# Kernel optimization log

Hardware: AMD Instinct MI355X
Metric: run time of the kernel (lower is better)

The kernel has to match this reference:

```python
import jax, jax.numpy as jnp
import numpy as np

MUL = 32          # channel multiplicity of every irrep
N_NODES = 50000
N_EDGES = 800000
SQRT2 = 1.4142135623730951
SQRT3 = 1.7320508075688772


def setup_inputs() -> dict:
    key = jax.random.key(0)
    k1, k2, k3, k4, k5 = jax.random.split(key, 5)
    x = jax.random.normal(k1, (N_NODES, 4 * MUL), dtype=jnp.float32)          # 32x0e + 32x1o
    edge_attr = jax.random.normal(k2, (N_EDGES, 4), dtype=jnp.float32)        # 1x0e + 1x1o
    edge_weight = jax.random.normal(k3, (N_EDGES, 5 * MUL), dtype=jnp.float32)  # 5 uvu paths
    edge_dst = jax.random.randint(k4, (N_EDGES,), 0, N_NODES, dtype=jnp.int64)
    edge_src = jax.random.randint(k5, (N_EDGES,), 0, N_NODES, dtype=jnp.int64)
    return {"x": x, "edge_attr": edge_attr, "edge_weight": edge_weight,
            "edge_dst": edge_dst, "edge_src": edge_src}


def _tp_scatter(x, edge_attr, edge_weight, edge_dst, edge_src):
    N = x.shape[0]
    E = edge_attr.shape[0]
    # split node features into l=0 scalars and l=1 vectors
    x0 = x[:, :MUL]                              # [N, 32]
    x1 = x[:, MUL:].reshape(N, MUL, 3)           # [N, 32, 3]
    a0 = edge_attr[:, :1]                        # [E, 1]
    a1 = edge_attr[:, 1:4]                       # [E, 3]
    w0, w1, w2, w3, w4 = [edge_weight[:, i * MUL:(i + 1) * MUL] for i in range(5)]

    xs0 = x0[edge_src]                           # [E, 32]  gather
    xs1 = x1[edge_src]                           # [E, 32, 3]

    # path 1: 0e x 0e -> 0e   (CG = 1, alpha = 1)
    o0 = w0 * xs0 * a0                                                   # [E, 32]
    # path 2: 0e x 1o -> 1o   (CG = delta/sqrt3, alpha = sqrt3 => net 1)
    o1 = (w1 * xs0)[:, :, None] * a1[:, None, :]                         # [E, 32, 3]
    # path 3: 1o x 0e -> 1o   (net coefficient 1)
    o2 = (w2[:, :, None] * xs1) * a0[:, :, None]                         # [E, 32, 3]
    # path 4: 1o x 1o -> 0e   (CG = delta/sqrt3, alpha = 1 => net 1/sqrt3)
    o3 = w3 * jnp.einsum('euk,ek->eu', xs1, a1) / SQRT3                  # [E, 32]
    # path 5: 1o x 1o -> 1e   (CG = eps/sqrt6, alpha = sqrt3 => net 1/sqrt2)
    o4 = w4[:, :, None] * jnp.cross(xs1, a1[:, None, :]) / SQRT2         # [E, 32, 3]

    edge_features = jnp.concatenate(
        [o0, o1.reshape(E, -1), o2.reshape(E, -1), o3, o4.reshape(E, -1)], axis=1)  # [E, 352]
    # scatter-add to destination nodes
    return jax.ops.segment_sum(edge_features, edge_dst, num_segments=N)  # [N, 352]


def reference(x, edge_attr, edge_weight, edge_dst, edge_src):
    return _tp_scatter(x, edge_attr, edge_weight, edge_dst, edge_src)
```

## Files before the change

### kernel.cpp

```cpp
#include <hip/hip_runtime.h>

#define MUL 32
#define N_NODES 50000
#define N_EDGES 800000
#define ROW_OUT 352
#define ROW_X 128
#define ROW_W 160

#define INV_SQRT3 0.57735026918962576f
#define INV_SQRT2 0.70710678118654752f

#define SCAN_THREADS 1024

__global__ __launch_bounds__(256) void hist_kernel(
    const int* __restrict__ edge_dst, int* __restrict__ counts)
{
    int e = blockIdx.x * blockDim.x + threadIdx.x;
    if (e < N_EDGES) atomicAdd(&counts[edge_dst[e]], 1);
}

__global__ __launch_bounds__(SCAN_THREADS) void scan_kernel(
    const int* __restrict__ counts, int* __restrict__ offsets,
    int* __restrict__ cursor)
{
    __shared__ int lds[SCAN_THREADS];
    const int t = threadIdx.x;
    int carry = 0;
    for (int base = 0; base < N_NODES; base += SCAN_THREADS) {
        int i = base + t;
        int v = (i < N_NODES) ? counts[i] : 0;
        lds[t] = v;
        __syncthreads();
        for (int off = 1; off < SCAN_THREADS; off <<= 1) {
            int add = (t >= off) ? lds[t - off] : 0;
            __syncthreads();
            lds[t] += add;
            __syncthreads();
        }
        int incl = lds[t];
        int excl = incl - v + carry;
        if (i < N_NODES) { offsets[i] = excl; cursor[i] = excl; }
        carry += lds[SCAN_THREADS - 1];
        __syncthreads();
    }
}

__global__ __launch_bounds__(256) void fill_kernel(
    const int* __restrict__ edge_dst, int* __restrict__ cursor,
    int* __restrict__ edge_ids)
{
    int e = blockIdx.x * blockDim.x + threadIdx.x;
    if (e < N_EDGES) {
        int p = atomicAdd(&cursor[edge_dst[e]], 1);
        edge_ids[p] = e;
    }
}

__global__ __launch_bounds__(256) void gather_kernel(
    const float* __restrict__ x,
    const float* __restrict__ edge_attr,
    const float* __restrict__ edge_weight,
    const int*   __restrict__ edge_src,
    const int*   __restrict__ offsets,
    const int*   __restrict__ counts,
    const int*   __restrict__ edge_ids,
    float*       __restrict__ out)
{
    const int wave_in_block = threadIdx.x >> 6;
    const int n = blockIdx.x * (blockDim.x >> 6) + wave_in_block;
    if (n >= N_NODES) return;

    const int lane = threadIdx.x & 63;
    const int half = lane >> 5;
    const int u = lane & 31;

    const int start = offsets[n];
    const int deg = counts[n];

    float acc0 = 0.f;
    float acc1x = 0.f, acc1y = 0.f, acc1z = 0.f;
    float acc2x = 0.f, acc2y = 0.f, acc2z = 0.f;
    float acc3 = 0.f;
    float acc4x = 0.f, acc4y = 0.f, acc4z = 0.f;

    for (int j = half; j < deg; j += 2) {
        const int e = edge_ids[start + j];
        const int src = edge_src[e];

        const float4 a = *reinterpret_cast<const float4*>(edge_attr + (size_t)e * 4);
        const float a0  = a.x;
        const float a1x = a.y, a1y = a.z, a1z = a.w;

        const float* wrow = edge_weight + (size_t)e * ROW_W;
        const float w0 = wrow[0 * MUL + u];
        const float w1 = wrow[1 * MUL + u];
        const float w2 = wrow[2 * MUL + u];
        const float w3 = wrow[3 * MUL + u];
        const float w4 = wrow[4 * MUL + u];

        const float* xrow = x + (size_t)src * ROW_X;
        const float xs0 = xrow[u];
        const float x1x = xrow[MUL + u * 3 + 0];
        const float x1y = xrow[MUL + u * 3 + 1];
        const float x1z = xrow[MUL + u * 3 + 2];

        acc0 += w0 * xs0 * a0;

        const float w1xs0 = w1 * xs0;
        acc1x += w1xs0 * a1x;
        acc1y += w1xs0 * a1y;
        acc1z += w1xs0 * a1z;

        const float w2a0 = w2 * a0;
        acc2x += w2a0 * x1x;
        acc2y += w2a0 * x1y;
        acc2z += w2a0 * x1z;

        const float dot = x1x * a1x + x1y * a1y + x1z * a1z;
        acc3 += w3 * dot * INV_SQRT3;

        const float cx = x1y * a1z - x1z * a1y;
        const float cy = x1z * a1x - x1x * a1z;
        const float cz = x1x * a1y - x1y * a1x;
        const float w4s = w4 * INV_SQRT2;
        acc4x += w4s * cx;
        acc4y += w4s * cy;
        acc4z += w4s * cz;
    }

    acc0  += __shfl_down(acc0, 32);
    acc1x += __shfl_down(acc1x, 32);
    acc1y += __shfl_down(acc1y, 32);
    acc1z += __shfl_down(acc1z, 32);
    acc2x += __shfl_down(acc2x, 32);
    acc2y += __shfl_down(acc2y, 32);
    acc2z += __shfl_down(acc2z, 32);
    acc3  += __shfl_down(acc3, 32);
    acc4x += __shfl_down(acc4x, 32);
    acc4y += __shfl_down(acc4y, 32);
    acc4z += __shfl_down(acc4z, 32);

    if (half == 0) {
        float* orow = out + (size_t)n * ROW_OUT;
        orow[u] = acc0;
        orow[1 * MUL + u * 3 + 0] = acc1x;
        orow[1 * MUL + u * 3 + 1] = acc1y;
        orow[1 * MUL + u * 3 + 2] = acc1z;
        orow[4 * MUL + u * 3 + 0] = acc2x;
        orow[4 * MUL + u * 3 + 1] = acc2y;
        orow[4 * MUL + u * 3 + 2] = acc2z;
        orow[7 * MUL + u] = acc3;
        orow[8 * MUL + u * 3 + 0] = acc4x;
        orow[8 * MUL + u * 3 + 1] = acc4y;
        orow[8 * MUL + u * 3 + 2] = acc4z;
    }
}

extern "C" void kernel_launch(void* const* d_in, const int* in_sizes, int n_in,
                              void* d_out, int out_size, void* d_ws, size_t ws_size,
                              hipStream_t stream) {
    const float* x           = (const float*)d_in[0];
    const float* edge_attr   = (const float*)d_in[1];
    const float* edge_weight = (const float*)d_in[2];
    const int*   edge_dst    = (const int*)d_in[3];
    const int*   edge_src    = (const int*)d_in[4];
    float* out = (float*)d_out;

    int* counts   = (int*)d_ws;
    int* offsets  = counts + N_NODES;
    int* cursor   = offsets + N_NODES;
    int* edge_ids = cursor + N_NODES;

    hipMemsetAsync(counts, 0, (size_t)N_NODES * sizeof(int), stream);

    const int eb = (N_EDGES + 255) / 256;
    hist_kernel<<<eb, 256, 0, stream>>>(edge_dst, counts);
    scan_kernel<<<1, SCAN_THREADS, 0, stream>>>(counts, offsets, cursor);
    fill_kernel<<<eb, 256, 0, stream>>>(edge_dst, cursor, edge_ids);

    const int waves_per_block = 4;
    const int nb = (N_NODES + waves_per_block - 1) / waves_per_block;
    gather_kernel<<<nb, waves_per_block * 64, 0, stream>>>(
        x, edge_attr, edge_weight, edge_src, offsets, counts, edge_ids, out);
}
```

Measured before the change: 914.9 us.

## Prefetch next edge, pack edge/src pairs, and use wave-shuffle scan

The single-block scan now uses wave-level shuffle scans with a small per-wave combine, replacing the LDS Hillis-Steele loop full of barriers, and it prefetches the next chunk of counts. The fill kernel stores (edge id, src) pairs, so the gather no longer does a dependent edge_src lookup. The gather loop software-pipelines by loading the next edge's data while computing the current one, and it reads edge weights with nontemporal loads. This costs more registers, which may lower occupancy.

```diff
diff --git a/kernel.cpp b/kernel.cpp
--- a/kernel.cpp
+++ b/kernel.cpp
@@ -23,47 +23,101 @@
     const int* __restrict__ counts, int* __restrict__ offsets,
     int* __restrict__ cursor)
 {
-    __shared__ int lds[SCAN_THREADS];
+    __shared__ int wsum[16];
+    __shared__ int wexcl[16];
+    __shared__ int blocktot;
+
     const int t = threadIdx.x;
+    const int w = t >> 6;
+    const int lane = t & 63;
+
     int carry = 0;
+    int v = (t < N_NODES) ? counts[t] : 0;
+
     for (int base = 0; base < N_NODES; base += SCAN_THREADS) {
-        int i = base + t;
-        int v = (i < N_NODES) ? counts[i] : 0;
-        lds[t] = v;
+        const int inext = base + SCAN_THREADS + t;
+        int vnext = (inext < N_NODES) ? counts[inext] : 0;
+
+        int s = v;
+        #pragma unroll
+        for (int off = 1; off < 64; off <<= 1) {
+            int y = __shfl_up(s, off);
+            if (lane >= off) s += y;
+        }
+        if (lane == 63) wsum[w] = s;
         __syncthreads();
-        for (int off = 1; off < SCAN_THREADS; off <<= 1) {
-            int add = (t >= off) ? lds[t - off] : 0;
-            __syncthreads();
-            lds[t] += add;
-            __syncthreads();
+
+        if (t < 16) {
+            int ws_ = wsum[t];
+            int ss = ws_;
+            #pragma unroll
+            for (int off = 1; off < 16; off <<= 1) {
+                int y = __shfl_up(ss, off);
+                if (t >= off) ss += y;
+            }
+            wexcl[t] = ss - ws_;
+            if (t == 15) blocktot = ss;
         }
-        int incl = lds[t];
-        int excl = incl - v + carry;
+        __syncthreads();
+
+        const int excl = s - v + wexcl[w] + carry;
+        const int i = base + t;
         if (i < N_NODES) { offsets[i] = excl; cursor[i] = excl; }
-        carry += lds[SCAN_THREADS - 1];
+        carry += blocktot;
+        v = vnext;
         __syncthreads();
     }
 }
 
 __global__ __launch_bounds__(256) void fill_kernel(
-    const int* __restrict__ edge_dst, int* __restrict__ cursor,
-    int* __restrict__ edge_ids)
+    const int* __restrict__ edge_dst, const int* __restrict__ edge_src,
+    int* __restrict__ cursor, int2* __restrict__ pairs)
 {
     int e = blockIdx.x * blockDim.x + threadIdx.x;
     if (e < N_EDGES) {
         int p = atomicAdd(&cursor[edge_dst[e]], 1);
-        edge_ids[p] = e;
-    }
+        pairs[p] = make_int2(e, edge_src[e]);
+    }
+}
+
+struct Ed {
+    float a0, a1x, a1y, a1z;
+    float w0, w1, w2, w3, w4;
+    float xs0, x1x, x1y, x1z;
+};
+
+__device__ __forceinline__ Ed load_edge(
+    const float* __restrict__ x,
+    const float* __restrict__ edge_attr,
+    const float* __restrict__ edge_weight,
+    int2 p, int u)
+{
+    Ed d;
+    const float4 a = *reinterpret_cast<const float4*>(edge_attr + (size_t)p.x * 4);
+    d.a0 = a.x; d.a1x = a.y; d.a1y = a.z; d.a1z = a.w;
+
+    const float* wrow = edge_weight + (size_t)p.x * ROW_W;
+    d.w0 = __builtin_nontemporal_load(wrow + 0 * MUL + u);
+    d.w1 = __builtin_nontemporal_load(wrow + 1 * MUL + u);
+    d.w2 = __builtin_nontemporal_load(wrow + 2 * MUL + u);
+    d.w3 = __builtin_nontemporal_load(wrow + 3 * MUL + u);
+    d.w4 = __builtin_nontemporal_load(wrow + 4 * MUL + u);
+
+    const float* xrow = x + (size_t)p.y * ROW_X;
+    d.xs0 = xrow[u];
+    d.x1x = xrow[MUL + u * 3 + 0];
+    d.x1y = xrow[MUL + u * 3 + 1];
+    d.x1z = xrow[MUL + u * 3 + 2];
+    return d;
 }
 
 __global__ __launch_bounds__(256) void gather_kernel(
     const float* __restrict__ x,
     const float* __restrict__ edge_attr,
     const float* __restrict__ edge_weight,
-    const int*   __restrict__ edge_src,
     const int*   __restrict__ offsets,
     const int*   __restrict__ counts,
-    const int*   __restrict__ edge_ids,
+    const int2*  __restrict__ pairs,
     float*       __restrict__ out)
 {
     const int wave_in_block = threadIdx.x >> 6;
@@ -83,49 +137,42 @@
     float acc3 = 0.f;
     float acc4x = 0.f, acc4y = 0.f, acc4z = 0.f;
 
-    for (int j = half; j < deg; j += 2) {
-        const int e = edge_ids[start + j];
-        const int src = edge_src[e];
-
-        const float4 a = *reinterpret_cast<const float4*>(edge_attr + (size_t)e * 4);
-        const float a0  = a.x;
-        const float a1x = a.y, a1y = a.z, a1z = a.w;
-
-        const float* wrow = edge_weight + (size_t)e * ROW_W;
-        const float w0 = wrow[0 * MUL + u];
-        const float w1 = wrow[1 * MUL + u];
-        const float w2 = wrow[2 * MUL + u];
-        const float w3 = wrow[3 * MUL + u];
-        const float w4 = wrow[4 * MUL + u];
-
-        const float* xrow = x + (size_t)src * ROW_X;
-        const float xs0 = xrow[u];
-        const float x1x = xrow[MUL + u * 3 + 0];
-        const float x1y = xrow[MUL + u * 3 + 1];
-        const float x1z = xrow[MUL + u * 3 + 2];
-
-        acc0 += w0 * xs0 * a0;
-
-        const float w1xs0 = w1 * xs0;
-        acc1x += w1xs0 * a1x;
-        acc1y += w1xs0 * a1y;
-        acc1z += w1xs0 * a1z;
-
-        const float w2a0 = w2 * a0;
-        acc2x += w2a0 * x1x;
-        acc2y += w2a0 * x1y;
-        acc2z += w2a0 * x1z;
-
-        const float dot = x1x * a1x + x1y * a1y + x1z * a1z;
-        acc3 += w3 * dot * INV_SQRT3;
-
-        const float cx = x1y * a1z - x1z * a1y;
-        const float cy = x1z * a1x - x1x * a1z;
-        const float cz = x1x * a1y - x1y * a1x;
-        const float w4s = w4 * INV_SQRT2;
-        acc4x += w4s * cx;
-        acc4y += w4s * cy;
-        acc4z += w4s * cz;
+    int j = half;
+    if (j < deg) {
+        int2 pcur = pairs[start + j];
+        int2 pnxt = (j + 2 < deg) ? pairs[start + j + 2] : pcur;
+        Ed dc = load_edge(x, edge_attr, edge_weight, pcur, u);
+
+        for (; j < deg; j += 2) {
+            int2 pfar = (j + 4 < deg) ? pairs[start + j + 4] : pnxt;
+            Ed dn = load_edge(x, edge_attr, edge_weight, pnxt, u);
+
+            acc0 += dc.w0 * dc.xs0 * dc.a0;
+
+            const float w1xs0 = dc.w1 * dc.xs0;
+            acc1x += w1xs0 * dc.a1x;
+            acc1y += w1xs0 * dc.a1y;
+            acc1z += w1xs0 * dc.a1z;
+
+            const float w2a0 = dc.w2 * dc.a0;
+            acc2x += w2a0 * dc.x1x;
+            acc2y += w2a0 * dc.x1y;
+            acc2z += w2a0 * dc.x1z;
+
+            const float dot = dc.x1x * dc.a1x + dc.x1y * dc.a1y + dc.x1z * dc.a1z;
+            acc3 += dc.w3 * dot * INV_SQRT3;
+
+            const float cx = dc.x1y * dc.a1z - dc.x1z * dc.a1y;
+            const float cy = dc.x1z * dc.a1x - dc.x1x * dc.a1z;
+            const float cz = dc.x1x * dc.a1y - dc.x1y * dc.a1x;
+            const float w4s = dc.w4 * INV_SQRT2;
+            acc4x += w4s * cx;
+            acc4y += w4s * cy;
+            acc4z += w4s * cz;
+
+            dc = dn;
+            pnxt = pfar;
+        }
     }
 
     acc0  += __shfl_down(acc0, 32);
@@ -166,20 +213,20 @@
     const int*   edge_src    = (const int*)d_in[4];
     float* out = (float*)d_out;
 
-    int* counts   = (int*)d_ws;
-    int* offsets  = counts + N_NODES;
-    int* cursor   = offsets + N_NODES;
-    int* edge_ids = cursor + N_NODES;
+    int*  counts  = (int*)d_ws;
+    int*  offsets = counts + N_NODES;
+    int*  cursor  = offsets + N_NODES;
+    int2* pairs   = (int2*)(cursor + N_NODES);
 
     hipMemsetAsync(counts, 0, (size_t)N_NODES * sizeof(int), stream);
 
     const int eb = (N_EDGES + 255) / 256;
     hist_kernel<<<eb, 256, 0, stream>>>(edge_dst, counts);
     scan_kernel<<<1, SCAN_THREADS, 0, stream>>>(counts, offsets, cursor);
-    fill_kernel<<<eb, 256, 0, stream>>>(edge_dst, cursor, edge_ids);
+    fill_kernel<<<eb, 256, 0, stream>>>(edge_dst, edge_src, cursor, pairs);
 
     const int waves_per_block = 4;
     const int nb = (N_NODES + waves_per_block - 1) / waves_per_block;
     gather_kernel<<<nb, waves_per_block * 64, 0, stream>>>(
-        x, edge_attr, edge_weight, edge_src, offsets, counts, edge_ids, out);
-}
+        x, edge_attr, edge_weight, offsets, counts, pairs, out);
+}
```

Result: faster. 868.5 us (-5.1%).
